# Kernel optimization log

Hardware: AMD Instinct MI355X
Metric: run time of the kernel (lower is better)

Reference implementation:

```python
import jax, jax.numpy as jnp
import numpy as np

SEQ_LEN, BATCH, VOCAB = 128, 32, 32000
EMB, HID = 32, 16


def setup_inputs() -> dict:
    key = jax.random.key(0)
    ks = jax.random.split(key, 10)
    return {
        "input_batch": jax.random.randint(ks[0], (SEQ_LEN, BATCH), 0, VOCAB, dtype=jnp.int64)
        if jax.config.jax_enable_x64 else jax.random.randint(ks[0], (SEQ_LEN, BATCH), 0, VOCAB, dtype=jnp.int32),
        "h0_lr": jax.random.uniform(ks[1], (BATCH, HID), dtype=jnp.float32),
        "h0_rl": jax.random.uniform(ks[2], (BATCH, HID), dtype=jnp.float32),
        "embedding": jax.random.normal(ks[3], (VOCAB, EMB), dtype=jnp.float32),
        "W_lr": jax.random.normal(ks[4], (HID, EMB + HID), dtype=jnp.float32) * 0.25,
        "b_lr": jax.random.normal(ks[5], (HID,), dtype=jnp.float32) * 0.25,
        "W_rl": jax.random.normal(ks[6], (HID, EMB + HID), dtype=jnp.float32) * 0.25,
        "b_rl": jax.random.normal(ks[7], (HID,), dtype=jnp.float32) * 0.25,
        "W_ho": jax.random.normal(ks[8], (VOCAB, 2 * HID), dtype=jnp.float32) * 0.25,
        "b_ho": jax.random.normal(ks[9], (VOCAB,), dtype=jnp.float32) * 0.25,
    }


def _rnn_step(W, b):
    # h_{t+1} = tanh([x_t, h_t] @ W^T + b)
    def f(h, x):
        h_new = jnp.tanh(jnp.concatenate([x, h], axis=-1) @ W.T + b)
        return h_new, h_new
    return f


def reference(input_batch, h0_lr, h0_rl, embedding, W_lr, b_lr, W_rl, b_rl, W_ho, b_ho):
    emb = embedding[input_batch]  # [S, B, EMB]
    # Left-to-right: consumes emb[0..S-2]; hLR[0] = h0_lr, len S
    _, hs_lr = jax.lax.scan(_rnn_step(W_lr, b_lr), h0_lr, emb[:-1])
    hLR = jnp.concatenate([h0_lr[None], hs_lr], axis=0)  # [S, B, HID]
    # Right-to-left: consumes emb[S-1 .. 1]; hRL[0] = h0_rl, len S
    _, hs_rl = jax.lax.scan(_rnn_step(W_rl, b_rl), h0_rl, emb[:0:-1])
    hRL = jnp.concatenate([h0_rl[None], hs_rl], axis=0)  # [S, B, HID]
    # prediction[i] pairs hLR[i] with hRL[S-1-i]
    combined = jnp.concatenate([hLR, hRL[::-1]], axis=-1)  # [S, B, 2*HID]
    logits = combined @ W_ho.T + b_ho  # [S, B, VOCAB]
    return jax.nn.log_softmax(logits, axis=-1)
```

## Files before the change

kernel.cpp:

```cpp
#include <hip/hip_runtime.h>
#include <hip/hip_bf16.h>
#include <math.h>

#define SS 128
#define BB 32
#define VV 32000
#define EE 32
#define HH 16
#define KK 32
#define NROWS (SS*BB)
#define NSL 16
#define VT 125

typedef __attribute__((ext_vector_type(4))) float f32x4;
typedef __attribute__((ext_vector_type(8))) short bf16x8;
typedef __attribute__((ext_vector_type(4))) short s16x4;

#define SWZ(h, r) __builtin_bit_cast(float, __builtin_amdgcn_ds_swizzle( \
    __builtin_bit_cast(int, (h)), ((r) << 10) | 0x1F))

__global__ __launch_bounds__(256) void k_prep(
    const float* __restrict__ Who, __hip_bfloat16* __restrict__ who_bf,
    const int* __restrict__ tok, const float* __restrict__ emb,
    const float* __restrict__ Wlr, const float* __restrict__ blr,
    const float* __restrict__ Wrl, const float* __restrict__ brl,
    float* __restrict__ xp) {
  if (blockIdx.x < 1000) {
    int i = blockIdx.x * 256 + threadIdx.x;
    f32x4 v = ((const f32x4*)Who)[i];
    s16x4 o;
    #pragma unroll
    for (int q = 0; q < 4; ++q) {
      __hip_bfloat16 h = __float2bfloat16(v[q]);
      o[q] = *reinterpret_cast<short*>(&h);
    }
    ((s16x4*)who_bf)[i] = o;
  } else {
    int g = (blockIdx.x - 1000) * 256 + threadIdx.x;
    int dir = g >> 16;
    int rem = g & 65535;
    int t = rem >> 9;
    int b = (rem >> 4) & 31;
    int j = rem & 15;
    const float* W  = dir ? Wrl : Wlr;
    const float* bv = dir ? brl : blr;
    int tk = tok[t*BB + b];
    const float* er = emb + tk*EE;
    const float* wr = W + j*(EE+HH);
    float acc = bv[j];
    #pragma unroll
    for (int k = 0; k < EE; ++k) acc += er[k] * wr[k];
    xp[g] = acc;
  }
}

__global__ __launch_bounds__(512) void k_rnn_fused(
    const float* __restrict__ xp,
    const float* __restrict__ h0lr, const float* __restrict__ h0rl,
    const float* __restrict__ Wlr, const float* __restrict__ Wrl,
    __hip_bfloat16* __restrict__ comb_bf) {
  int dir = blockIdx.x;
  int tid = threadIdx.x;
  int b = tid >> 4;
  int j = tid & 15;
  const float* W  = dir ? Wrl : Wlr;
  const float* h0 = dir ? h0rl : h0lr;
  float wr[HH];
  #pragma unroll
  for (int r = 0; r < HH; ++r) wr[r] = W[j*(EE+HH) + EE + (j ^ r)];
  const float* x = xp + dir * (SS*BB*HH);
  float h = h0[b*HH + j];
  if (dir == 0) comb_bf[0*(BB*KK) + b*KK + j] = __float2bfloat16(h);
  else          comb_bf[(SS-1)*(BB*KK) + b*KK + HH + j] = __float2bfloat16(h);
  int xoff  = dir ? ((SS-1)*BB*HH + tid) : tid;
  int xstep = dir ? -(BB*HH) : (BB*HH);
  float xcur = x[xoff];
  for (int t = 1; t < SS; ++t) {
    float xnext = (t < SS-1) ? x[xoff + xstep] : 0.f;
    xoff += xstep;
    float t1 = SWZ(h, 1),  t2 = SWZ(h, 2),  t3 = SWZ(h, 3),  t4 = SWZ(h, 4);
    float t5 = SWZ(h, 5),  t6 = SWZ(h, 6),  t7 = SWZ(h, 7),  t8 = SWZ(h, 8);
    float t9 = SWZ(h, 9),  t10 = SWZ(h, 10), t11 = SWZ(h, 11), t12 = SWZ(h, 12);
    float t13 = SWZ(h, 13), t14 = SWZ(h, 14), t15 = SWZ(h, 15);
    float a0 = fmaf(wr[0], h,  xcur);
    a0 = fmaf(wr[4],  t4,  a0);
    a0 = fmaf(wr[8],  t8,  a0);
    a0 = fmaf(wr[12], t12, a0);
    float a1 = wr[1] * t1;
    a1 = fmaf(wr[5],  t5,  a1);
    a1 = fmaf(wr[9],  t9,  a1);
    a1 = fmaf(wr[13], t13, a1);
    float a2 = wr[2] * t2;
    a2 = fmaf(wr[6],  t6,  a2);
    a2 = fmaf(wr[10], t10, a2);
    a2 = fmaf(wr[14], t14, a2);
    float a3 = wr[3] * t3;
    a3 = fmaf(wr[7],  t7,  a3);
    a3 = fmaf(wr[11], t11, a3);
    a3 = fmaf(wr[15], t15, a3);
    float acc = (a0 + a1) + (a2 + a3);
    float e = __expf(2.f * acc);
    h = 1.f - 2.f / (e + 1.f);
    int ci = dir ? ((SS-1-t)*(BB*KK) + b*KK + HH + j)
                 : (t*(BB*KK) + b*KK + j);
    comb_bf[ci] = __float2bfloat16(h);
    xcur = xnext;
  }
}

__global__ __launch_bounds__(256) void k_sumexp(
    const __hip_bfloat16* __restrict__ cb, const __hip_bfloat16* __restrict__ wb,
    const float* __restrict__ bho, float* __restrict__ part) {
  int w = blockIdx.x * 4 + (threadIdx.x >> 6);
  int lane = threadIdx.x & 63;
  int rt = w >> 4;
  int sl = w & 15;
  int v0 = sl * (VT*16);
  int g = lane >> 4, c = lane & 15;
  bf16x8 bfr = *(const bf16x8*)(cb + (size_t)(rt*16 + c)*KK + g*8);
  float s = 0.f;
  for (int t = 0; t < VT; ++t) {
    int v = v0 + t*16;
    bf16x8 af = *(const bf16x8*)(wb + (size_t)(v + c)*KK + g*8);
    f32x4 bh = *(const f32x4*)(bho + v + g*4);
    f32x4 d = __builtin_amdgcn_mfma_f32_16x16x32_bf16(af, bfr, bh, 0, 0, 0);
    s += __expf(d[0]) + __expf(d[1]) + __expf(d[2]) + __expf(d[3]);
  }
  s += __shfl_xor(s, 16);
  s += __shfl_xor(s, 32);
  if (lane < 16)
    part[(size_t)(rt*16 + lane)*NSL + sl] = s;
}

__global__ __launch_bounds__(256) void k_write(
    const __hip_bfloat16* __restrict__ cb, const __hip_bfloat16* __restrict__ wb,
    const float* __restrict__ bho, const float* __restrict__ part,
    float* __restrict__ out) {
  int w = blockIdx.x * 4 + (threadIdx.x >> 6);
  int lane = threadIdx.x & 63;
  int rt = w >> 4;
  int sl = w & 15;
  int v0 = sl * (VT*16);
  int g = lane >> 4, c = lane & 15;
  size_t row = rt*16 + c;
  const f32x4* pp = (const f32x4*)(part + row*NSL);
  f32x4 p0 = pp[0], p1 = pp[1], p2 = pp[2], p3 = pp[3];
  float s = (p0[0]+p0[1]+p0[2]+p0[3]) + (p1[0]+p1[1]+p1[2]+p1[3])
          + (p2[0]+p2[1]+p2[2]+p2[3]) + (p3[0]+p3[1]+p3[2]+p3[3]);
  float Lr = logf(s);
  bf16x8 bfr = *(const bf16x8*)(cb + row*KK + g*8);
  for (int t = 0; t < VT; ++t) {
    int v = v0 + t*16;
    bf16x8 af = *(const bf16x8*)(wb + (size_t)(v + c)*KK + g*8);
    f32x4 bh = *(const f32x4*)(bho + v + g*4);
    f32x4 cin = bh - Lr;
    f32x4 d = __builtin_amdgcn_mfma_f32_16x16x32_bf16(af, bfr, cin, 0, 0, 0);
    *(f32x4*)(out + row*VV + v + g*4) = d;
  }
}

extern "C" void kernel_launch(void* const* d_in, const int* in_sizes, int n_in,
                              void* d_out, int out_size, void* d_ws, size_t ws_size,
                              hipStream_t stream) {
  const int*   tok  = (const int*)d_in[0];
  const float* h0lr = (const float*)d_in[1];
  const float* h0rl = (const float*)d_in[2];
  const float* emb  = (const float*)d_in[3];
  const float* Wlr  = (const float*)d_in[4];
  const float* blr  = (const float*)d_in[5];
  const float* Wrl  = (const float*)d_in[6];
  const float* brl  = (const float*)d_in[7];
  const float* Who  = (const float*)d_in[8];
  const float* bho  = (const float*)d_in[9];
  float* out = (float*)d_out;
  float* ws  = (float*)d_ws;

  float* xp   = ws;
  float* part = ws + 131072;
  __hip_bfloat16* comb_bf = (__hip_bfloat16*)(ws + 196608);
  __hip_bfloat16* who_bf  = (__hip_bfloat16*)(ws + 262144);

  hipLaunchKernelGGL(k_prep, dim3(1512), dim3(256), 0, stream,
                     Who, who_bf, tok, emb, Wlr, blr, Wrl, brl, xp);
  hipLaunchKernelGGL(k_rnn_fused, dim3(2), dim3(512), 0, stream,
                     xp, h0lr, h0rl, Wlr, Wrl, comb_bf);
  hipLaunchKernelGGL(k_sumexp, dim3(1024), dim3(256), 0, stream,
                     comb_bf, who_bf, bho, part);
  hipLaunchKernelGGL(k_write, dim3(1024), dim3(256), 0, stream,
                     comb_bf, who_bf, bho, part, out);
}
```

Before: 220.3 us.

## Use DPP lane exchanges in RNN, split RNN across blocks, swizzle GEMM block order

The recurrent step now does its intra-16-lane exchanges with DPP quad permutes and row mirrors instead of ds_swizzle, which goes through the LDS crossbar and has higher latency on the serial dependency chain. The RNN launch is also split from two 512-thread blocks into eight 128-thread blocks, so each sequential chain runs on its own CU with fewer waves per block. Separately, the sumexp and write kernels remap blockIdx so consecutive blocks spread across slices, changing how work lands on XCDs and caches. The DPP mapping must reproduce exactly the XOR permutation the swizzle gave, and a mismatch would silently give wrong results.

```diff
diff --git a/kernel.cpp b/kernel.cpp
--- a/kernel.cpp
+++ b/kernel.cpp
@@ -16,8 +16,8 @@
 typedef __attribute__((ext_vector_type(8))) short bf16x8;
 typedef __attribute__((ext_vector_type(4))) short s16x4;
 
-#define SWZ(h, r) __builtin_bit_cast(float, __builtin_amdgcn_ds_swizzle( \
-    __builtin_bit_cast(int, (h)), ((r) << 10) | 0x1F))
+#define DPPF(x, ctrl) __builtin_bit_cast(float, __builtin_amdgcn_update_dpp( \
+    __builtin_bit_cast(int, (x)), __builtin_bit_cast(int, (x)), (ctrl), 0xF, 0xF, false))
 
 __global__ __launch_bounds__(256) void k_prep(
     const float* __restrict__ Who, __hip_bfloat16* __restrict__ who_bf,
@@ -54,15 +54,15 @@
   }
 }
 
-__global__ __launch_bounds__(512) void k_rnn_fused(
+__global__ __launch_bounds__(128) void k_rnn_fused(
     const float* __restrict__ xp,
     const float* __restrict__ h0lr, const float* __restrict__ h0rl,
     const float* __restrict__ Wlr, const float* __restrict__ Wrl,
     __hip_bfloat16* __restrict__ comb_bf) {
-  int dir = blockIdx.x;
-  int tid = threadIdx.x;
-  int b = tid >> 4;
-  int j = tid & 15;
+  int bid = blockIdx.x;
+  int dir = bid >> 2;
+  int b = (bid & 3) * 8 + (threadIdx.x >> 4);
+  int j = threadIdx.x & 15;
   const float* W  = dir ? Wrl : Wlr;
   const float* h0 = dir ? h0rl : h0lr;
   float wr[HH];
@@ -72,16 +72,27 @@
   float h = h0[b*HH + j];
   if (dir == 0) comb_bf[0*(BB*KK) + b*KK + j] = __float2bfloat16(h);
   else          comb_bf[(SS-1)*(BB*KK) + b*KK + HH + j] = __float2bfloat16(h);
-  int xoff  = dir ? ((SS-1)*BB*HH + tid) : tid;
+  int xoff  = dir ? ((SS-1)*BB*HH + b*HH + j) : (b*HH + j);
   int xstep = dir ? -(BB*HH) : (BB*HH);
   float xcur = x[xoff];
   for (int t = 1; t < SS; ++t) {
     float xnext = (t < SS-1) ? x[xoff + xstep] : 0.f;
     xoff += xstep;
-    float t1 = SWZ(h, 1),  t2 = SWZ(h, 2),  t3 = SWZ(h, 3),  t4 = SWZ(h, 4);
-    float t5 = SWZ(h, 5),  t6 = SWZ(h, 6),  t7 = SWZ(h, 7),  t8 = SWZ(h, 8);
-    float t9 = SWZ(h, 9),  t10 = SWZ(h, 10), t11 = SWZ(h, 11), t12 = SWZ(h, 12);
-    float t13 = SWZ(h, 13), t14 = SWZ(h, 14), t15 = SWZ(h, 15);
+    float t1  = DPPF(h, 0xB1);
+    float t2  = DPPF(h, 0x4E);
+    float t3  = DPPF(h, 0x1B);
+    float t7  = DPPF(h, 0x141);
+    float t15 = DPPF(h, 0x140);
+    float t4  = DPPF(t7, 0x1B);
+    float t5  = DPPF(t7, 0x4E);
+    float t6  = DPPF(t7, 0xB1);
+    float t8  = DPPF(t15, 0x141);
+    float t12 = DPPF(t15, 0x1B);
+    float t13 = DPPF(t15, 0x4E);
+    float t14 = DPPF(t15, 0xB1);
+    float t9  = DPPF(t8, 0xB1);
+    float t10 = DPPF(t8, 0x4E);
+    float t11 = DPPF(t8, 0x1B);
     float a0 = fmaf(wr[0], h,  xcur);
     a0 = fmaf(wr[4],  t4,  a0);
     a0 = fmaf(wr[8],  t8,  a0);
@@ -111,7 +122,8 @@
 __global__ __launch_bounds__(256) void k_sumexp(
     const __hip_bfloat16* __restrict__ cb, const __hip_bfloat16* __restrict__ wb,
     const float* __restrict__ bho, float* __restrict__ part) {
-  int w = blockIdx.x * 4 + (threadIdx.x >> 6);
+  int wg = ((blockIdx.x & 7) << 7) | (blockIdx.x >> 3);
+  int w = wg * 4 + (threadIdx.x >> 6);
   int lane = threadIdx.x & 63;
   int rt = w >> 4;
   int sl = w & 15;
@@ -136,7 +148,8 @@
     const __hip_bfloat16* __restrict__ cb, const __hip_bfloat16* __restrict__ wb,
     const float* __restrict__ bho, const float* __restrict__ part,
     float* __restrict__ out) {
-  int w = blockIdx.x * 4 + (threadIdx.x >> 6);
+  int wg = ((blockIdx.x & 7) << 7) | (blockIdx.x >> 3);
+  int w = wg * 4 + (threadIdx.x >> 6);
   int lane = threadIdx.x & 63;
   int rt = w >> 4;
   int sl = w & 15;
@@ -182,7 +195,7 @@
 
   hipLaunchKernelGGL(k_prep, dim3(1512), dim3(256), 0, stream,
                      Who, who_bf, tok, emb, Wlr, blr, Wrl, brl, xp);
-  hipLaunchKernelGGL(k_rnn_fused, dim3(2), dim3(512), 0, stream,
+  hipLaunchKernelGGL(k_rnn_fused, dim3(8), dim3(128), 0, stream,
                      xp, h0lr, h0rl, Wlr, Wrl, comb_bf);
   hipLaunchKernelGGL(k_sumexp, dim3(1024), dim3(256), 0, stream,
                      comb_bf, who_bf, bho, part);
```

After: 222.1 us. Within noise of the previous version (+0.8%).
